# Performance work log

Hardware: AMD Instinct MI355X
Metric: run time of the kernel (lower is better)

The kernel has to match this reference:

```python
import jax, jax.numpy as jnp
import numpy as np

VOCAB = 1024
EMBED = 256
HIDDEN = 512
MAX_LEN = 32
TEMP = 1.0
BATCH = 2048


def setup_inputs() -> dict:
    key = jax.random.key(0)
    ks = jax.random.split(key, 11)
    s = 0.02  # small init scale for weights
    return dict(
        x=jax.random.normal(ks[0], (BATCH, HIDDEN), dtype=jnp.float32),
        gumbel=jax.random.gumbel(ks[1], (MAX_LEN, BATCH, VOCAB), dtype=jnp.float32),
        W_ih=jax.random.normal(ks[2], (4 * HIDDEN, EMBED), dtype=jnp.float32) * s,
        W_hh=jax.random.normal(ks[3], (4 * HIDDEN, HIDDEN), dtype=jnp.float32) * s,
        b_ih=jax.random.normal(ks[4], (4 * HIDDEN,), dtype=jnp.float32) * s,
        b_hh=jax.random.normal(ks[5], (4 * HIDDEN,), dtype=jnp.float32) * s,
        W_out=jax.random.normal(ks[6], (VOCAB, HIDDEN), dtype=jnp.float32) * s,
        b_out=jax.random.normal(ks[7], (VOCAB,), dtype=jnp.float32) * s,
        W_emb=jax.random.normal(ks[8], (EMBED, VOCAB), dtype=jnp.float32) * s,
        b_emb=jax.random.normal(ks[9], (EMBED,), dtype=jnp.float32) * s,
        sos=jax.random.normal(ks[10], (EMBED,), dtype=jnp.float32) * 0.01,
    )


def reference(x, gumbel, W_ih, W_hh, b_ih, b_hh, W_out, b_out, W_emb, b_emb, sos):
    B = x.shape[0]
    h0 = x                                   # prev_hidden = input features
    c0 = jnp.zeros_like(x)
    e0 = jnp.broadcast_to(sos, (B, EMBED))   # SOS embedding

    def step(carry, g):
        h, c, e = carry
        # torch LSTMCell gate order: i, f, g, o
        gates = e @ W_ih.T + b_ih + h @ W_hh.T + b_hh   # [B, 4H]
        i, f, gg, o = jnp.split(gates, 4, axis=-1)
        i = jax.nn.sigmoid(i)
        f = jax.nn.sigmoid(f)
        gg = jnp.tanh(gg)
        o = jax.nn.sigmoid(o)
        c_new = f * c + i * gg
        h_new = o * jnp.tanh(c_new)
        logits = h_new @ W_out.T + b_out                # [B, V]
        # RelaxedOneHotCategorical rsample: softmax((logits + Gumbel)/temp)
        x_s = jax.nn.softmax((logits + g) / TEMP, axis=-1)
        e_new = x_s @ W_emb.T + b_emb                   # [B, E]
        return (h_new, c_new, e_new), x_s

    _, seq = jax.lax.scan(step, (h0, c0, e0), gumbel)   # [L, B, V]
    seq = jnp.transpose(seq, (1, 0, 2))                 # [B, L, V]
    eos = jnp.zeros((B, 1, VOCAB), seq.dtype).at[:, 0, 0].set(1.0)
    return jnp.concatenate([seq, eos], axis=1)          # [B, L+1, V]
```

## Files before the change

### kernel.cpp

```cpp
#include <hip/hip_runtime.h>
#include <hip/hip_bf16.h>

#define B_   2048
#define V_   1024
#define H_   512
#define E_   256
#define L_   32

typedef __attribute__((ext_vector_type(4))) float f32x4;
typedef unsigned short u16;
typedef unsigned int   u32;
typedef unsigned char  u8;
typedef unsigned long long u64;
typedef long long      i64;

__device__ __forceinline__ u32 f32b(float x){ union{float f;u32 u;}v; v.f=x; return v.u; }
__device__ __forceinline__ float bf32(u32 u){ union{float f;u32 u;}v; v.u=u; return v.f; }
__device__ __forceinline__ u16 f2bf(float x) {
    u32 u = f32b(x);
    u32 r = u + 0x7fffu + ((u >> 16) & 1u);
    return (u16)(r >> 16);
}
__device__ __forceinline__ u8 f2e4m3(float x) {
    u32 u = f32b(x);
    u32 s = (u >> 24) & 0x80u;
    u32 a = u & 0x7fffffffu;
    if (a < 0x3c800000u) return (u8)s;
    if (a > 0x43e00000u) a = 0x43e00000u;
    u32 r = a + 0x000fffffu + ((a >> 20) & 1u);
    if (r > 0x43e00000u) r = 0x43e00000u;
    u32 ex = (r >> 23) - 120u;
    u32 mn = (r >> 20) & 7u;
    return (u8)(s | (ex << 3) | mn);
}
__device__ __forceinline__ u8 f2fp8(float x) {
#if __has_builtin(__builtin_amdgcn_cvt_pk_fp8_f32)
    return (u8)(__builtin_amdgcn_cvt_pk_fp8_f32(x, x, 0, false) & 0xff);
#else
    return f2e4m3(x);
#endif
}
__device__ __forceinline__ float sig_(float x)  { return 1.f / (1.f + __expf(-x)); }
__device__ __forceinline__ float tanh_(float x) { return 1.f - 2.f / (__expf(2.f * x) + 1.f); }

__device__ __forceinline__ void ag_st64(void* p, u64 v) {
    __hip_atomic_store((u64*)p, v, __ATOMIC_RELAXED, __HIP_MEMORY_SCOPE_AGENT);
}
__device__ __forceinline__ u64 ag_ld64(const void* p) {
    return __hip_atomic_load((const u64*)p, __ATOMIC_RELAXED, __HIP_MEMORY_SCOPE_AGENT);
}
__device__ __forceinline__ void ag_st32(void* p, u32 v) {
    __hip_atomic_store((u32*)p, v, __ATOMIC_RELAXED, __HIP_MEMORY_SCOPE_AGENT);
}
__device__ __forceinline__ u32 ag_ld32(const void* p) {
    return __hip_atomic_load((const u32*)p, __ATOMIC_RELAXED, __HIP_MEMORY_SCOPE_AGENT);
}

__global__ void prep(const float* __restrict__ W_ih, const float* __restrict__ W_hh,
                     const float* __restrict__ b_ih, const float* __restrict__ b_hh,
                     const float* __restrict__ W_out, const float* __restrict__ W_emb,
                     u8* __restrict__ w1f, u8* __restrict__ wof, u8* __restrict__ wef,
                     float* __restrict__ b1, u32* __restrict__ flg)
{
    int idx = blockIdx.x * 256 + threadIdx.x;
    if (idx < 1572864) {
        int e = idx & 7, l = (idx >> 3) & 63, jj = (idx >> 9) & 1, wv = (idx >> 10) & 7,
            g = (idx >> 13) & 3;
        int rest = idx >> 15;
        int hb = rest / 24, ks = rest % 24;
        int k = ks * 32 + ((l >> 4) << 3) + e;
        int row = g * 512 + hb * 256 + wv * 32 + jj * 16 + (l & 15);
        float v = (k < E_) ? W_ih[row * E_ + k] : W_hh[row * H_ + (k - E_)];
        w1f[idx] = f2e4m3(v * 64.f);
    } else if (idx < 2097152) {
        int j = idx - 1572864;
        int e = j & 7, l = (j >> 3) & 63, jj = (j >> 9) & 1, wv = (j >> 10) & 7,
            vh2 = (j >> 13) & 1, ks = (j >> 14) & 15, hb = j >> 18;
        int k = ks * 32 + ((l >> 4) << 3) + e;
        int v = hb * 512 + vh2 * 256 + wv * 32 + jj * 16 + (l & 15);
        wof[j] = f2e4m3(W_out[v * H_ + k] * 64.f);
    } else if (idx < 2359296) {
        int j = idx - 2097152;
        int e = j & 7, l = (j >> 3) & 63, jj = (j >> 9) & 1, wv = (j >> 10) & 7,
            ksp = (j >> 13) & 15, hb = j >> 17;
        int kv = hb * 512 + ksp * 32 + ((l >> 4) << 3) + e;
        int ce = wv * 32 + jj * 16 + (l & 15);
        wef[j] = f2e4m3(W_emb[ce * V_ + kv] * 64.f);
    } else if (idx < 2361344) {
        int j = idx - 2359296;
        b1[j] = b_ih[j] + b_hh[j];
    } else if (idx < 2365440) {
        flg[idx - 2361344] = 0u;
    }
}

#define AEO   131072u
#define XSO   143488u
#define RMX   151808u
#define RSM   152320u
#define LDS_TOTAL 152832

#define WAITVM_(N) asm volatile("s_waitcnt vmcnt(" #N ")" ::: "memory")
#define WAITVM(N) WAITVM_(N)

typedef const __attribute__((address_space(1))) void* gvp;
typedef __attribute__((address_space(3))) void* svp;

__device__ __forceinline__ void pbar(u32* myf, u32* pef, u32 n, u32 tid) {
    asm volatile("s_waitcnt vmcnt(0)" ::: "memory");
    __syncthreads();
    if (tid == 0) {
        __hip_atomic_fetch_add(myf, 1u, __ATOMIC_RELAXED, __HIP_MEMORY_SCOPE_AGENT);
        while (__hip_atomic_load(pef, __ATOMIC_RELAXED, __HIP_MEMORY_SCOPE_AGENT) < n)
            __builtin_amdgcn_s_sleep(2);
    }
    __syncthreads();
}

__global__ __launch_bounds__(512, 2)
void lstm_fused(const float* __restrict__ x, const float* __restrict__ gum,
                const u8* __restrict__ w1f, const u8* __restrict__ wof,
                const u8* __restrict__ wef, const float* __restrict__ b1,
                const float* __restrict__ b_out, const float* __restrict__ b_emb,
                const float* __restrict__ sos, float* __restrict__ out,
                u8* __restrict__ hx, char* __restrict__ ms, char* __restrict__ ep,
                u32* __restrict__ flg)
{
    extern __shared__ char smem[];

    const u32 tid = threadIdx.x;
    const u32 w   = tid >> 6;
    const u32 l   = tid & 63u;
    const u32 q   = l >> 4;
    const u32 col = l & 15u;

    const u32 bid = blockIdx.x;
    const u32 p   = bid & 127u;
    const u32 hb  = bid >> 7;
    const u32 ph  = 1u - hb;
    const int r0  = (int)(p << 4);

    u32* myf = flg + p * 32u + hb * 16u;
    u32* pef = flg + p * 32u + ph * 16u;
    u32 nbar = 0;

    const u32 wK  = w << 10;
    const u32 lB  = l << 4;
    const u32 l8  = l << 3;
    const u32 q8  = q << 3;
    const u32 colB776 = col * 776u;
    const u32 colB520 = col * 520u;

    const char* w1p = (const char*)w1f + (size_t)hb * 786432u;
    const char* wop = (const char*)wof + (size_t)hb * 262144u;
    const char* wep = (const char*)wef + (size_t)hb * 131072u;

#define ISS(BASE, C) do { u32 _c = (u32)(C); \
    u32 _o = (u32)__builtin_amdgcn_readfirstlane((int)(((_c & 15u) << 13) + wK)); \
    __builtin_amdgcn_global_load_lds((gvp)((BASE) + ((size_t)_c << 13) + wK + lB), \
                                     (svp)(smem + _o), 16, 0, 0); } while (0)

#define CONSA(G, C) { const char* _fb = smem + (((u32)(C) & 15u) << 13) + wK + l8; \
    acc[G][0] = __builtin_amdgcn_mfma_f32_16x16x32_fp8_fp8(a8, *(const i64*)(_fb), acc[G][0], 0, 0, 0); \
    acc[G][1] = __builtin_amdgcn_mfma_f32_16x16x32_fp8_fp8(a8, *(const i64*)(_fb + 512u), acc[G][1], 0, 0, 0); }

#define CONSB(V2, C, A8) { const char* _fb = smem + (((u32)(C) & 15u) << 13) + wK + l8; \
    accB[V2][0] = __builtin_amdgcn_mfma_f32_16x16x32_fp8_fp8(A8, *(const i64*)(_fb), accB[V2][0], 0, 0, 0); \
    accB[V2][1] = __builtin_amdgcn_mfma_f32_16x16x32_fp8_fp8(A8, *(const i64*)(_fb + 512u), accB[V2][1], 0, 0, 0); }

#define CONSC(C) { const char* _fb = smem + (((u32)(C) & 15u) << 13) + wK + l8; \
    i64 _x = *(const i64*)(smem + XSO + colB520 + (((u32)(C)) << 5) + q8); \
    accC[0] = __builtin_amdgcn_mfma_f32_16x16x32_fp8_fp8(_x, *(const i64*)(_fb), accC[0], 0, 0, 0); \
    accC[1] = __builtin_amdgcn_mfma_f32_16x16x32_fp8_fp8(_x, *(const i64*)(_fb + 512u), accC[1], 0, 0, 0); }

    for (u32 i = tid; i < 16u * 512u; i += 512u) {
        u32 row = i >> 9, vl = i & 511u;
        __builtin_nontemporal_store((hb == 0u && vl == 0u) ? 1.f : 0.f,
            &out[((size_t)(r0 + (int)row) * 33 + 32) * V_ + hb * 512u + vl]);
    }
    for (u32 i = tid; i < 16u * 256u; i += 512u) {
        u32 row = i >> 8, k = i & 255u;
        *(u8*)(smem + AEO + row * 776u + k) = f2fp8(sos[k] * 16.f);
    }
    for (u32 i = tid; i < 16u * 512u; i += 512u) {
        u32 row = i >> 9, k = i & 511u;
        *(u8*)(smem + AEO + row * 776u + 256u + k) = f2fp8(x[(r0 + (int)row) * H_ + k] * 16.f);
    }

    float bia[2], bfa[2], bga[2], boa[2];
    #pragma unroll
    for (int jj = 0; jj < 2; ++jj) {
        int jg = (int)(hb * 256u + (w << 5) + ((u32)jj << 4) + col);
        bia[jj] = b1[jg];           bfa[jj] = b1[H_ + jg];
        bga[jj] = b1[2 * H_ + jg];  boa[jj] = b1[3 * H_ + jg];
    }
    float bov[2][2];
    #pragma unroll
    for (int v2 = 0; v2 < 2; ++v2)
        #pragma unroll
        for (int jj = 0; jj < 2; ++jj)
            bov[v2][jj] = b_out[hb * 512u + (u32)v2 * 256u + (w << 5) + ((u32)jj << 4) + col];
    float bem16[2];
    #pragma unroll
    for (int jj = 0; jj < 2; ++jj)
        bem16[jj] = b_emb[(w << 5) + ((u32)jj << 4) + col] * 16.f;

    float creg[2][4];
    #pragma unroll
    for (int jj = 0; jj < 2; ++jj)
        #pragma unroll
        for (int r = 0; r < 4; ++r) creg[jj][r] = 0.f;

    __syncthreads();

    const f32x4 fz = {0.f, 0.f, 0.f, 0.f};
    const float S1 = 1.f / 1024.f;

    ISS(w1p, 0);  ISS(w1p, 1);  ISS(w1p, 2);  ISS(w1p, 3);  ISS(w1p, 4);
    ISS(w1p, 5);  ISS(w1p, 6);  ISS(w1p, 7);  ISS(w1p, 8);  ISS(w1p, 9);
    ISS(w1p, 10); ISS(w1p, 11); ISS(w1p, 12); ISS(w1p, 13); ISS(w1p, 14);

    #pragma unroll 1
    for (int t = 0; t < L_; ++t) {
        f32x4 acc[4][2];
        #pragma unroll
        for (int g = 0; g < 4; ++g) { acc[g][0] = fz; acc[g][1] = fz; }

        #pragma unroll 1
        for (int ks = 0; ks < 20; ++ks) {
            i64 a8 = *(const i64*)(smem + AEO + colB776 + ((u32)ks << 5) + q8);
            int c0 = ks << 2;
            WAITVM(11);
            CONSA(0, c0); CONSA(1, c0 + 1); CONSA(2, c0 + 2); CONSA(3, c0 + 3);
            ISS(w1p, c0 + 15); ISS(w1p, c0 + 16); ISS(w1p, c0 + 17); ISS(w1p, c0 + 18);
        }
        {   i64 a8 = *(const i64*)(smem + AEO + colB776 + (20u << 5) + q8);
            WAITVM(11); CONSA(0, 80); CONSA(1, 81); CONSA(2, 82); CONSA(3, 83); ISS(w1p, 95); }
        {   i64 a8 = *(const i64*)(smem + AEO + colB776 + (21u << 5) + q8);
            WAITVM(8);  CONSA(0, 84); CONSA(1, 85); CONSA(2, 86); CONSA(3, 87); }
        {   i64 a8 = *(const i64*)(smem + AEO + colB776 + (22u << 5) + q8);
            WAITVM(4);  CONSA(0, 88); CONSA(1, 89); CONSA(2, 90); CONSA(3, 91); }
        {   i64 a8 = *(const i64*)(smem + AEO + colB776 + (23u << 5) + q8);
            WAITVM(0);  CONSA(0, 92); CONSA(1, 93); CONSA(2, 94); CONSA(3, 95); }
        __syncthreads();

        #pragma unroll
        for (int jj = 0; jj < 2; ++jj) {
            u32 jg = hb * 256u + (w << 5) + ((u32)jj << 4) + col;
            #pragma unroll
            for (int r = 0; r < 4; ++r) {
                float gi = sig_(acc[0][jj][r] * S1 + bia[jj]);
                float gf = sig_(acc[1][jj][r] * S1 + bfa[jj]);
                float gg = tanh_(acc[2][jj][r] * S1 + bga[jj]);
                float go = sig_(acc[3][jj][r] * S1 + boa[jj]);
                float c  = gf * creg[jj][r] + gi * gg;
                creg[jj][r] = c;
                float h = go * tanh_(c);
                *(u8*)(smem + AEO + ((q << 2) + (u32)r) * 776u + 256u + jg) = f2fp8(h * 16.f);
            }
        }
        __syncthreads();

        {   u32 row = tid >> 5, off = (tid & 31u) << 3;
            u64 v = *(const u64*)(smem + AEO + row * 776u + 256u + hb * 256u + off);
            ag_st64(hx + (size_t)p * 8192u + row * 512u + hb * 256u + off, v);
        }
        ISS(wop, 0);  ISS(wop, 1);  ISS(wop, 2);  ISS(wop, 3);  ISS(wop, 4);
        ISS(wop, 5);  ISS(wop, 6);  ISS(wop, 7);  ISS(wop, 8);  ISS(wop, 9);
        ISS(wop, 10); ISS(wop, 11); ISS(wop, 12); ISS(wop, 13); ISS(wop, 14);
        const float* gt = gum + (size_t)t * (B_ * V_) + (size_t)r0 * V_;
        float gr[2][2][4];
        #pragma unroll
        for (int v2 = 0; v2 < 2; ++v2)
            #pragma unroll
            for (int jj = 0; jj < 2; ++jj) {
                u32 vg = hb * 512u + (u32)v2 * 256u + (w << 5) + ((u32)jj << 4) + col;
                #pragma unroll
                for (int r = 0; r < 4; ++r)
                    gr[v2][jj][r] = __builtin_nontemporal_load(&gt[((q << 2) + (u32)r) * V_ + vg]);
            }
        ++nbar; pbar(myf, pef, nbar, tid);
        {   u32 row = tid >> 5, off = (tid & 31u) << 3;
            u64 v = ag_ld64(hx + (size_t)p * 8192u + row * 512u + ph * 256u + off);
            *(u64*)(smem + AEO + row * 776u + 256u + ph * 256u + off) = v;
        }
        __syncthreads();

        f32x4 accB[2][2];
        accB[0][0] = fz; accB[0][1] = fz; accB[1][0] = fz; accB[1][1] = fz;
        #pragma unroll 1
        for (int g = 0; g < 4; ++g) {
            i64 a80 = *(const i64*)(smem + AEO + colB776 + 256u + (((u32)g << 1) << 5) + q8);
            i64 a81 = *(const i64*)(smem + AEO + colB776 + 256u + ((((u32)g << 1) | 1u) << 5) + q8);
            int c0 = g << 2;
            WAITVM(11);
            CONSB(0, c0, a80); CONSB(1, c0 + 1, a80);
            CONSB(0, c0 + 2, a81); CONSB(1, c0 + 3, a81);
            ISS(wop, c0 + 15); ISS(wop, c0 + 16); ISS(wop, c0 + 17); ISS(wop, c0 + 18);
        }
        {   i64 a80 = *(const i64*)(smem + AEO + colB776 + 256u + (8u << 5) + q8);
            i64 a81 = *(const i64*)(smem + AEO + colB776 + 256u + (9u << 5) + q8);
            WAITVM(11); CONSB(0, 16, a80); CONSB(1, 17, a80); CONSB(0, 18, a81); CONSB(1, 19, a81);
            ISS(wop, 31); }
        {   i64 a80 = *(const i64*)(smem + AEO + colB776 + 256u + (10u << 5) + q8);
            i64 a81 = *(const i64*)(smem + AEO + colB776 + 256u + (11u << 5) + q8);
            WAITVM(8);  CONSB(0, 20, a80); CONSB(1, 21, a80); CONSB(0, 22, a81); CONSB(1, 23, a81); }
        {   i64 a80 = *(const i64*)(smem + AEO + colB776 + 256u + (12u << 5) + q8);
            i64 a81 = *(const i64*)(smem + AEO + colB776 + 256u + (13u << 5) + q8);
            WAITVM(4);  CONSB(0, 24, a80); CONSB(1, 25, a80); CONSB(0, 26, a81); CONSB(1, 27, a81); }
        {   i64 a80 = *(const i64*)(smem + AEO + colB776 + 256u + (14u << 5) + q8);
            i64 a81 = *(const i64*)(smem + AEO + colB776 + 256u + (15u << 5) + q8);
            WAITVM(0);  CONSB(0, 28, a80); CONSB(1, 29, a80); CONSB(0, 30, a81); CONSB(1, 31, a81); }

        float m_loc[4], s_loc[4];
        #pragma unroll
        for (int r = 0; r < 4; ++r) m_loc[r] = -1e30f;
        #pragma unroll
        for (int v2 = 0; v2 < 2; ++v2)
            #pragma unroll
            for (int jj = 0; jj < 2; ++jj)
                #pragma unroll
                for (int r = 0; r < 4; ++r) {
                    float zz = accB[v2][jj][r] * S1 + bov[v2][jj] + gr[v2][jj][r];
                    accB[v2][jj][r] = zz;
                    m_loc[r] = fmaxf(m_loc[r], zz);
                }
        #pragma unroll
        for (int m = 1; m < 16; m <<= 1)
            #pragma unroll
            for (int r = 0; r < 4; ++r) m_loc[r] = fmaxf(m_loc[r], __shfl_xor(m_loc[r], m, 64));
        if (col == 0) {
            #pragma unroll
            for (int r = 0; r < 4; ++r)
                *(float*)(smem + RMX + ((((q << 2) + (u32)r) << 3) + w) * 4u) = m_loc[r];
        }
        __syncthreads();
        #pragma unroll
        for (int r = 0; r < 4; ++r) {
            float mm = -1e30f;
            #pragma unroll
            for (int ww = 0; ww < 8; ++ww)
                mm = fmaxf(mm, *(const float*)(smem + RMX + ((((q << 2) + (u32)r) << 3) + (u32)ww) * 4u));
            m_loc[r] = mm;
        }
        ISS(wep, 0);  ISS(wep, 1);  ISS(wep, 2);  ISS(wep, 3);  ISS(wep, 4);
        ISS(wep, 5);  ISS(wep, 6);  ISS(wep, 7);  ISS(wep, 8);  ISS(wep, 9);
        ISS(wep, 10); ISS(wep, 11); ISS(wep, 12); ISS(wep, 13); ISS(wep, 14);
        float ps[4] = {0.f, 0.f, 0.f, 0.f};
        #pragma unroll
        for (int v2 = 0; v2 < 2; ++v2)
            #pragma unroll
            for (int jj = 0; jj < 2; ++jj) {
                u32 vl = (u32)v2 * 256u + (w << 5) + ((u32)jj << 4) + col;
                #pragma unroll
                for (int r = 0; r < 4; ++r) {
                    float Ee = __expf(accB[v2][jj][r] - m_loc[r]);
                    accB[v2][jj][r] = Ee;
                    ps[r] += Ee;
                    *(u8*)(smem + XSO + ((q << 2) + (u32)r) * 520u + vl) = f2fp8(Ee * 256.f);
                }
            }
        #pragma unroll
        for (int m = 1; m < 16; m <<= 1)
            #pragma unroll
            for (int r = 0; r < 4; ++r) ps[r] += __shfl_xor(ps[r], m, 64);
        if (col == 0) {
            #pragma unroll
            for (int r = 0; r < 4; ++r)
                *(float*)(smem + RSM + ((((q << 2) + (u32)r) << 3) + w) * 4u) = ps[r];
        }
        __syncthreads();
        #pragma unroll
        for (int r = 0; r < 4; ++r) {
            float ss = 0.f;
            #pragma unroll
            for (int ww = 0; ww < 8; ++ww)
                ss += *(const float*)(smem + RSM + ((((q << 2) + (u32)r) << 3) + (u32)ww) * 4u);
            s_loc[r] = ss;
        }

        f32x4 accC[2];
        accC[0] = fz; accC[1] = fz;
        WAITVM(11); CONSC(0);  CONSC(1);  CONSC(2);  CONSC(3);  ISS(wep, 15);
        WAITVM(8);  CONSC(4);  CONSC(5);  CONSC(6);  CONSC(7);
        WAITVM(4);  CONSC(8);  CONSC(9);  CONSC(10); CONSC(11);
        WAITVM(0);  CONSC(12); CONSC(13); CONSC(14); CONSC(15);

        float part[2][4];
        #pragma unroll
        for (int jj = 0; jj < 2; ++jj)
            #pragma unroll
            for (int r = 0; r < 4; ++r)
                part[jj][r] = accC[jj][r] * (16.f / 16384.f);
        if (w == 0 && col == 0) {
            #pragma unroll
            for (int r = 0; r < 4; ++r) {
                u64 v = ((u64)f32b(s_loc[r]) << 32) | (u64)f32b(m_loc[r]);
                ag_st64(ms + (size_t)p * 256u + hb * 128u + (((q << 2) + (u32)r) << 3), v);
            }
        }
        #pragma unroll
        for (int r = 0; r < 4; ++r) {
            u32 row = (q << 2) + (u32)r;
            u32 pv = (u32)f2bf(part[0][r]) | ((u32)f2bf(part[1][r]) << 16);
            ag_st32(ep + (size_t)p * 16384u + hb * 8192u + (((row << 3) + w) << 6) + (col << 2), pv);
        }
        ISS(w1p, 0);  ISS(w1p, 1);  ISS(w1p, 2);  ISS(w1p, 3);  ISS(w1p, 4);
        ISS(w1p, 5);  ISS(w1p, 6);  ISS(w1p, 7);  ISS(w1p, 8);  ISS(w1p, 9);
        ISS(w1p, 10); ISS(w1p, 11); ISS(w1p, 12); ISS(w1p, 13); ISS(w1p, 14);
        ++nbar; pbar(myf, pef, nbar, tid);

        float f0a[4], f1a[4], inva[4];
        #pragma unroll
        for (int r = 0; r < 4; ++r) {
            u64 v = ag_ld64(ms + (size_t)p * 256u + ph * 128u + (((q << 2) + (u32)r) << 3));
            float m_p = bf32((u32)v), s_p = bf32((u32)(v >> 32));
            float mg = fmaxf(m_loc[r], m_p);
            float f0 = __expf(m_loc[r] - mg), f1 = __expf(m_p - mg);
            float inv = 1.f / (s_loc[r] * f0 + s_p * f1);
            f0a[r] = f0; f1a[r] = f1; inva[r] = inv;
        }
        #pragma unroll
        for (int v2 = 0; v2 < 2; ++v2)
            #pragma unroll
            for (int jj = 0; jj < 2; ++jj) {
                u32 vg = hb * 512u + (u32)v2 * 256u + (w << 5) + ((u32)jj << 4) + col;
                #pragma unroll
                for (int r = 0; r < 4; ++r)
                    __builtin_nontemporal_store(accB[v2][jj][r] * f0a[r] * inva[r],
                        &out[((size_t)(r0 + (int)((q << 2) + (u32)r)) * 33 + t) * V_ + vg]);
            }
        #pragma unroll
        for (int r = 0; r < 4; ++r) {
            u32 row = (q << 2) + (u32)r;
            u32 pv = ag_ld32(ep + (size_t)p * 16384u + ph * 8192u + (((row << 3) + w) << 6) + (col << 2));
            #pragma unroll
            for (int jj = 0; jj < 2; ++jj) {
                float pe = bf32(((pv >> (16 * jj)) & 0xffffu) << 16);
                float e16 = (part[jj][r] * f0a[r] + pe * f1a[r]) * inva[r] + bem16[jj];
                *(u8*)(smem + AEO + row * 776u + (w << 5) + ((u32)jj << 4) + col) = f2fp8(e16);
            }
        }
        __syncthreads();
    }
#undef ISS
#undef CONSA
#undef CONSB
#undef CONSC
}

extern "C" void kernel_launch(void* const* d_in, const int* in_sizes, int n_in,
                              void* d_out, int out_size, void* d_ws, size_t ws_size,
                              hipStream_t stream) {
    const float* x     = (const float*)d_in[0];
    const float* gum   = (const float*)d_in[1];
    const float* W_ih  = (const float*)d_in[2];
    const float* W_hh  = (const float*)d_in[3];
    const float* b_ih  = (const float*)d_in[4];
    const float* b_hh  = (const float*)d_in[5];
    const float* W_out = (const float*)d_in[6];
    const float* b_out = (const float*)d_in[7];
    const float* W_emb = (const float*)d_in[8];
    const float* b_emb = (const float*)d_in[9];
    const float* sos   = (const float*)d_in[10];
    float* out = (float*)d_out;

    char* ws = (char*)d_ws;
    u8*    w1f = (u8*)(ws);
    u8*    wof = (u8*)(ws + 1572864);
    u8*    wef = (u8*)(ws + 2097152);
    float* b1  = (float*)(ws + 2359296);
    u32*   flg = (u32*)(ws + 2367488);
    u8*    hx  = (u8*)(ws + 2383872);
    char*  ms  = (char*)(ws + 3432448);
    char*  ep  = (char*)(ws + 3465216);

    hipFuncSetAttribute((const void*)lstm_fused,
                        hipFuncAttributeMaxDynamicSharedMemorySize, LDS_TOTAL);

    prep<<<9240, 256, 0, stream>>>(W_ih, W_hh, b_ih, b_hh, W_out, W_emb,
                                   w1f, wof, wef, b1, flg);
    lstm_fused<<<256, 512, LDS_TOTAL, stream>>>(x, gum, w1f, wof, wef, b1,
                                                b_out, b_emb, sos, out,
                                                hx, ms, ep, flg);
}
```

Measured before the change: 868.1 us.

## Split output projection into own-half and peer-half phases around pair barrier

The output-logits GEMM over the hidden dimension is split so the block first consumes the W_out chunks matching its own locally computed hidden half before the inter-block pair barrier. Only after that does it wait for and import the peer's hidden half and finish the peer chunks. The barrier wait now uses a partial vmcnt so outstanding weight prefetches are not drained. Scheduling barriers pin the issue order. This overlaps barrier latency with MFMA work, at the cost of reordered weight chunks that must match the preprocessed layout, and a relaxed wait that must still cover the global stores before signalling.

```diff
diff --git a/kernel.cpp b/kernel.cpp
--- a/kernel.cpp
+++ b/kernel.cpp
@@ -102,20 +102,10 @@
 
 #define WAITVM_(N) asm volatile("s_waitcnt vmcnt(" #N ")" ::: "memory")
 #define WAITVM(N) WAITVM_(N)
+#define SCHEDB() __builtin_amdgcn_sched_barrier(0)
 
 typedef const __attribute__((address_space(1))) void* gvp;
 typedef __attribute__((address_space(3))) void* svp;
-
-__device__ __forceinline__ void pbar(u32* myf, u32* pef, u32 n, u32 tid) {
-    asm volatile("s_waitcnt vmcnt(0)" ::: "memory");
-    __syncthreads();
-    if (tid == 0) {
-        __hip_atomic_fetch_add(myf, 1u, __ATOMIC_RELAXED, __HIP_MEMORY_SCOPE_AGENT);
-        while (__hip_atomic_load(pef, __ATOMIC_RELAXED, __HIP_MEMORY_SCOPE_AGENT) < n)
-            __builtin_amdgcn_s_sleep(2);
-    }
-    __syncthreads();
-}
 
 __global__ __launch_bounds__(512, 2)
 void lstm_fused(const float* __restrict__ x, const float* __restrict__ gum,
@@ -150,23 +140,46 @@
     const u32 q8  = q << 3;
     const u32 colB776 = col * 776u;
     const u32 colB520 = col * 520u;
+    const u32 hb16 = hb << 4, ph16 = ph << 4;
+    const u32 hOwnOff  = 256u + (hb << 8);
+    const u32 hPeerOff = 256u + (ph << 8);
 
     const char* w1p = (const char*)w1f + (size_t)hb * 786432u;
     const char* wop = (const char*)wof + (size_t)hb * 262144u;
     const char* wep = (const char*)wef + (size_t)hb * 131072u;
+
+#define PBAR(N) do { WAITVM(N); __syncthreads(); \
+    if (tid == 0) { \
+        __hip_atomic_fetch_add(myf, 1u, __ATOMIC_RELAXED, __HIP_MEMORY_SCOPE_AGENT); \
+        while (__hip_atomic_load(pef, __ATOMIC_RELAXED, __HIP_MEMORY_SCOPE_AGENT) < nbar) \
+            __builtin_amdgcn_s_sleep(2); \
+    } \
+    __syncthreads(); } while (0)
 
 #define ISS(BASE, C) do { u32 _c = (u32)(C); \
     u32 _o = (u32)__builtin_amdgcn_readfirstlane((int)(((_c & 15u) << 13) + wK)); \
     __builtin_amdgcn_global_load_lds((gvp)((BASE) + ((size_t)_c << 13) + wK + lB), \
                                      (svp)(smem + _o), 16, 0, 0); } while (0)
+#define ISSB_OWN(I) do { u32 _c = hb16 + (u32)(I); \
+    u32 _o = (u32)__builtin_amdgcn_readfirstlane((int)((((u32)(I) & 15u) << 13) + wK)); \
+    __builtin_amdgcn_global_load_lds((gvp)(wop + ((size_t)_c << 13) + wK + lB), \
+                                     (svp)(smem + _o), 16, 0, 0); } while (0)
+#define ISSB_P(I) do { u32 _c = ph16 + (u32)(I); \
+    u32 _o = (u32)__builtin_amdgcn_readfirstlane((int)((((u32)(I) & 15u) << 13) + wK)); \
+    __builtin_amdgcn_global_load_lds((gvp)(wop + ((size_t)_c << 13) + wK + lB), \
+                                     (svp)(smem + _o), 16, 0, 0); } while (0)
 
 #define CONSA(G, C) { const char* _fb = smem + (((u32)(C) & 15u) << 13) + wK + l8; \
     acc[G][0] = __builtin_amdgcn_mfma_f32_16x16x32_fp8_fp8(a8, *(const i64*)(_fb), acc[G][0], 0, 0, 0); \
     acc[G][1] = __builtin_amdgcn_mfma_f32_16x16x32_fp8_fp8(a8, *(const i64*)(_fb + 512u), acc[G][1], 0, 0, 0); }
 
-#define CONSB(V2, C, A8) { const char* _fb = smem + (((u32)(C) & 15u) << 13) + wK + l8; \
+#define CONSB(V2, SLOT, A8) { const char* _fb = smem + (((u32)(SLOT) & 15u) << 13) + wK + l8; \
     accB[V2][0] = __builtin_amdgcn_mfma_f32_16x16x32_fp8_fp8(A8, *(const i64*)(_fb), accB[V2][0], 0, 0, 0); \
     accB[V2][1] = __builtin_amdgcn_mfma_f32_16x16x32_fp8_fp8(A8, *(const i64*)(_fb + 512u), accB[V2][1], 0, 0, 0); }
+
+#define BGRP(I, NW, HOFF) { \
+    i64 a8 = *(const i64*)(smem + AEO + colB776 + (HOFF) + ((u32)(I) << 5) + q8); \
+    WAITVM(NW); CONSB(0, 2*(I), a8); CONSB(1, 2*(I) + 1, a8); }
 
 #define CONSC(C) { const char* _fb = smem + (((u32)(C) & 15u) << 13) + wK + l8; \
     i64 _x = *(const i64*)(smem + XSO + colB520 + (((u32)(C)) << 5) + q8); \
@@ -265,9 +278,12 @@
             u64 v = *(const u64*)(smem + AEO + row * 776u + 256u + hb * 256u + off);
             ag_st64(hx + (size_t)p * 8192u + row * 512u + hb * 256u + off, v);
         }
-        ISS(wop, 0);  ISS(wop, 1);  ISS(wop, 2);  ISS(wop, 3);  ISS(wop, 4);
-        ISS(wop, 5);  ISS(wop, 6);  ISS(wop, 7);  ISS(wop, 8);  ISS(wop, 9);
-        ISS(wop, 10); ISS(wop, 11); ISS(wop, 12); ISS(wop, 13); ISS(wop, 14);
+        SCHEDB();
+        ISSB_OWN(0);  ISSB_OWN(1);  ISSB_OWN(2);  ISSB_OWN(3);
+        ISSB_OWN(4);  ISSB_OWN(5);  ISSB_OWN(6);  ISSB_OWN(7);
+        ISSB_OWN(8);  ISSB_OWN(9);  ISSB_OWN(10); ISSB_OWN(11);
+        ISSB_OWN(12); ISSB_OWN(13); ISSB_OWN(14); ISSB_OWN(15);
+        SCHEDB();
         const float* gt = gum + (size_t)t * (B_ * V_) + (size_t)r0 * V_;
         float gr[2][2][4];
         #pragma unroll
@@ -279,38 +295,36 @@
                 for (int r = 0; r < 4; ++r)
                     gr[v2][jj][r] = __builtin_nontemporal_load(&gt[((q << 2) + (u32)r) * V_ + vg]);
             }
-        ++nbar; pbar(myf, pef, nbar, tid);
-        {   u32 row = tid >> 5, off = (tid & 31u) << 3;
-            u64 v = ag_ld64(hx + (size_t)p * 8192u + row * 512u + ph * 256u + off);
-            *(u64*)(smem + AEO + row * 776u + 256u + ph * 256u + off) = v;
-        }
-        __syncthreads();
+        SCHEDB();
 
         f32x4 accB[2][2];
         accB[0][0] = fz; accB[0][1] = fz; accB[1][0] = fz; accB[1][1] = fz;
-        #pragma unroll 1
-        for (int g = 0; g < 4; ++g) {
-            i64 a80 = *(const i64*)(smem + AEO + colB776 + 256u + (((u32)g << 1) << 5) + q8);
-            i64 a81 = *(const i64*)(smem + AEO + colB776 + 256u + ((((u32)g << 1) | 1u) << 5) + q8);
-            int c0 = g << 2;
-            WAITVM(11);
-            CONSB(0, c0, a80); CONSB(1, c0 + 1, a80);
-            CONSB(0, c0 + 2, a81); CONSB(1, c0 + 3, a81);
-            ISS(wop, c0 + 15); ISS(wop, c0 + 16); ISS(wop, c0 + 17); ISS(wop, c0 + 18);
-        }
-        {   i64 a80 = *(const i64*)(smem + AEO + colB776 + 256u + (8u << 5) + q8);
-            i64 a81 = *(const i64*)(smem + AEO + colB776 + 256u + (9u << 5) + q8);
-            WAITVM(11); CONSB(0, 16, a80); CONSB(1, 17, a80); CONSB(0, 18, a81); CONSB(1, 19, a81);
-            ISS(wop, 31); }
-        {   i64 a80 = *(const i64*)(smem + AEO + colB776 + 256u + (10u << 5) + q8);
-            i64 a81 = *(const i64*)(smem + AEO + colB776 + 256u + (11u << 5) + q8);
-            WAITVM(8);  CONSB(0, 20, a80); CONSB(1, 21, a80); CONSB(0, 22, a81); CONSB(1, 23, a81); }
-        {   i64 a80 = *(const i64*)(smem + AEO + colB776 + 256u + (12u << 5) + q8);
-            i64 a81 = *(const i64*)(smem + AEO + colB776 + 256u + (13u << 5) + q8);
-            WAITVM(4);  CONSB(0, 24, a80); CONSB(1, 25, a80); CONSB(0, 26, a81); CONSB(1, 27, a81); }
-        {   i64 a80 = *(const i64*)(smem + AEO + colB776 + 256u + (14u << 5) + q8);
-            i64 a81 = *(const i64*)(smem + AEO + colB776 + 256u + (15u << 5) + q8);
-            WAITVM(0);  CONSB(0, 28, a80); CONSB(1, 29, a80); CONSB(0, 30, a81); CONSB(1, 31, a81); }
+        BGRP(0, 44, hOwnOff); BGRP(1, 40, hOwnOff);
+        BGRP(2, 36, hOwnOff); BGRP(3, 32, hOwnOff);
+        BGRP(4, 28, hOwnOff); BGRP(5, 24, hOwnOff);
+        BGRP(6, 20, hOwnOff); BGRP(7, 16, hOwnOff);
+
+        ++nbar; PBAR(16);
+
+        u64 himp;
+        {   u32 row = tid >> 5, off = (tid & 31u) << 3;
+            himp = ag_ld64(hx + (size_t)p * 8192u + row * 512u + ph * 256u + off);
+        }
+        SCHEDB();
+        ISSB_P(0);  ISSB_P(1);  ISSB_P(2);  ISSB_P(3);
+        ISSB_P(4);  ISSB_P(5);  ISSB_P(6);  ISSB_P(7);
+        ISSB_P(8);  ISSB_P(9);  ISSB_P(10); ISSB_P(11);
+        ISSB_P(12); ISSB_P(13); ISSB_P(14); ISSB_P(15);
+        SCHEDB();
+        {   u32 row = tid >> 5, off = (tid & 31u) << 3;
+            *(u64*)(smem + AEO + row * 776u + 256u + ph * 256u + off) = himp;
+        }
+        __syncthreads();
+
+        BGRP(0, 28, hPeerOff); BGRP(1, 24, hPeerOff);
+        BGRP(2, 20, hPeerOff); BGRP(3, 16, hPeerOff);
+        BGRP(4, 12, hPeerOff); BGRP(5, 8, hPeerOff);
+        BGRP(6, 4, hPeerOff);  BGRP(7, 0, hPeerOff);
 
         float m_loc[4], s_loc[4];
         #pragma unroll
@@ -405,10 +419,12 @@
             u32 pv = (u32)f2bf(part[0][r]) | ((u32)f2bf(part[1][r]) << 16);
             ag_st32(ep + (size_t)p * 16384u + hb * 8192u + (((row << 3) + w) << 6) + (col << 2), pv);
         }
+        SCHEDB();
         ISS(w1p, 0);  ISS(w1p, 1);  ISS(w1p, 2);  ISS(w1p, 3);  ISS(w1p, 4);
         ISS(w1p, 5);  ISS(w1p, 6);  ISS(w1p, 7);  ISS(w1p, 8);  ISS(w1p, 9);
         ISS(w1p, 10); ISS(w1p, 11); ISS(w1p, 12); ISS(w1p, 13); ISS(w1p, 14);
-        ++nbar; pbar(myf, pef, nbar, tid);
+        SCHEDB();
+        ++nbar; PBAR(30);
 
         float f0a[4], f1a[4], inva[4];
         #pragma unroll
@@ -444,9 +460,13 @@
         __syncthreads();
     }
 #undef ISS
+#undef ISSB_OWN
+#undef ISSB_P
 #undef CONSA
 #undef CONSB
+#undef BGRP
 #undef CONSC
+#undef PBAR
 }
 
 extern "C" void kernel_launch(void* const* d_in, const int* in_sizes, int n_in,
```

After: 990.8 us. 1.14x slower.

## Stream fp8 weights directly into registers instead of staging through LDS

Applied to the files above, without the earlier changes.

Replaces the global_load_lds ring buffer (16 slots of 8KB in LDS) with a six-deep register ring of 16-byte weight loads that feed the MFMAs directly. LDS drops from about 150KB to about 21KB and becomes static shared memory. The prep kernel's weight layout is reordered so that each lane reads a contiguous 16-byte chunk. The Wout prefetch now starts before the cross-block barrier, so the hidden-state exchange overlaps with those loads. The trade-off is higher register pressure and reliance on the compiler's vmcnt scheduling instead of explicit waits.

```diff
diff --git a/kernel.cpp b/kernel.cpp
--- a/kernel.cpp
+++ b/kernel.cpp
@@ -8,6 +8,7 @@
 #define L_   32
 
 typedef __attribute__((ext_vector_type(4))) float f32x4;
+typedef __attribute__((ext_vector_type(2))) long i64x2;
 typedef unsigned short u16;
 typedef unsigned int   u32;
 typedef unsigned char  u8;
@@ -62,60 +63,56 @@
                      u8* __restrict__ w1f, u8* __restrict__ wof, u8* __restrict__ wef,
                      float* __restrict__ b1, u32* __restrict__ flg)
 {
-    int idx = blockIdx.x * 256 + threadIdx.x;
-    if (idx < 1572864) {
-        int e = idx & 7, l = (idx >> 3) & 63, jj = (idx >> 9) & 1, wv = (idx >> 10) & 7,
-            g = (idx >> 13) & 3;
-        int rest = idx >> 15;
-        int hb = rest / 24, ks = rest % 24;
-        int k = ks * 32 + ((l >> 4) << 3) + e;
-        int row = g * 512 + hb * 256 + wv * 32 + jj * 16 + (l & 15);
+    u32 idx = blockIdx.x * 256 + threadIdx.x;
+    if (idx < 1572864u) {
+        u32 hb = idx / 786432u;
+        u32 r  = idx - hb * 786432u;
+        u32 ks = r >> 15;
+        u32 r2 = r & 32767u;
+        u32 g = r2 >> 13, wv = (r2 >> 10) & 7u, l = (r2 >> 4) & 63u,
+            jj = (r2 >> 3) & 1u, e = r2 & 7u;
+        u32 k = ks * 32u + ((l >> 4) << 3) + e;
+        u32 row = g * 512u + hb * 256u + wv * 32u + jj * 16u + (l & 15u);
         float v = (k < E_) ? W_ih[row * E_ + k] : W_hh[row * H_ + (k - E_)];
         w1f[idx] = f2e4m3(v * 64.f);
-    } else if (idx < 2097152) {
-        int j = idx - 1572864;
-        int e = j & 7, l = (j >> 3) & 63, jj = (j >> 9) & 1, wv = (j >> 10) & 7,
-            vh2 = (j >> 13) & 1, ks = (j >> 14) & 15, hb = j >> 18;
-        int k = ks * 32 + ((l >> 4) << 3) + e;
-        int v = hb * 512 + vh2 * 256 + wv * 32 + jj * 16 + (l & 15);
+    } else if (idx < 2097152u) {
+        u32 j = idx - 1572864u;
+        u32 hb = j >> 18;
+        u32 r  = j & 262143u;
+        u32 ks = r >> 14;
+        u32 r2 = r & 16383u;
+        u32 vh2 = r2 >> 13;
+        u32 r3 = r2 & 8191u;
+        u32 wv = r3 >> 10, l = (r3 >> 4) & 63u, jj = (r3 >> 3) & 1u, e = r3 & 7u;
+        u32 k = ks * 32u + ((l >> 4) << 3) + e;
+        u32 v = hb * 512u + vh2 * 256u + wv * 32u + jj * 16u + (l & 15u);
         wof[j] = f2e4m3(W_out[v * H_ + k] * 64.f);
-    } else if (idx < 2359296) {
-        int j = idx - 2097152;
-        int e = j & 7, l = (j >> 3) & 63, jj = (j >> 9) & 1, wv = (j >> 10) & 7,
-            ksp = (j >> 13) & 15, hb = j >> 17;
-        int kv = hb * 512 + ksp * 32 + ((l >> 4) << 3) + e;
-        int ce = wv * 32 + jj * 16 + (l & 15);
+    } else if (idx < 2359296u) {
+        u32 j = idx - 2097152u;
+        u32 hb = j >> 17;
+        u32 r  = j & 131071u;
+        u32 ksp = r >> 13;
+        u32 r2 = r & 8191u;
+        u32 wv = r2 >> 10, l = (r2 >> 4) & 63u, jj = (r2 >> 3) & 1u, e = r2 & 7u;
+        u32 kv = hb * 512u + ksp * 32u + ((l >> 4) << 3) + e;
+        u32 ce = wv * 32u + jj * 16u + (l & 15u);
         wef[j] = f2e4m3(W_emb[ce * V_ + kv] * 64.f);
-    } else if (idx < 2361344) {
-        int j = idx - 2359296;
+    } else if (idx < 2361344u) {
+        u32 j = idx - 2359296u;
         b1[j] = b_ih[j] + b_hh[j];
-    } else if (idx < 2365440) {
-        flg[idx - 2361344] = 0u;
-    }
-}
-
-#define AEO   131072u
-#define XSO   143488u
-#define RMX   151808u
-#define RSM   152320u
-#define LDS_TOTAL 152832
+    } else if (idx < 2365440u) {
+        flg[idx - 2361344u] = 0u;
+    }
+}
+
+#define AEO   0u
+#define XSO   12416u
+#define RMX   20736u
+#define RSM   21248u
+#define LDS_TOTAL 21760
 
 #define WAITVM_(N) asm volatile("s_waitcnt vmcnt(" #N ")" ::: "memory")
 #define WAITVM(N) WAITVM_(N)
-
-typedef const __attribute__((address_space(1))) void* gvp;
-typedef __attribute__((address_space(3))) void* svp;
-
-__device__ __forceinline__ void pbar(u32* myf, u32* pef, u32 n, u32 tid) {
-    asm volatile("s_waitcnt vmcnt(0)" ::: "memory");
-    __syncthreads();
-    if (tid == 0) {
-        __hip_atomic_fetch_add(myf, 1u, __ATOMIC_RELAXED, __HIP_MEMORY_SCOPE_AGENT);
-        while (__hip_atomic_load(pef, __ATOMIC_RELAXED, __HIP_MEMORY_SCOPE_AGENT) < n)
-            __builtin_amdgcn_s_sleep(2);
-    }
-    __syncthreads();
-}
 
 __global__ __launch_bounds__(512, 2)
 void lstm_fused(const float* __restrict__ x, const float* __restrict__ gum,
@@ -126,7 +123,7 @@
                 u8* __restrict__ hx, char* __restrict__ ms, char* __restrict__ ep,
                 u32* __restrict__ flg)
 {
-    extern __shared__ char smem[];
+    __shared__ __align__(16) char smem[LDS_TOTAL];
 
     const u32 tid = threadIdx.x;
     const u32 w   = tid >> 6;
@@ -144,34 +141,26 @@
     u32* pef = flg + p * 32u + ph * 16u;
     u32 nbar = 0;
 
-    const u32 wK  = w << 10;
-    const u32 lB  = l << 4;
-    const u32 l8  = l << 3;
+    const u32 wvl = (w << 10) + (l << 4);
     const u32 q8  = q << 3;
     const u32 colB776 = col * 776u;
     const u32 colB520 = col * 520u;
 
-    const char* w1p = (const char*)w1f + (size_t)hb * 786432u;
-    const char* wop = (const char*)wof + (size_t)hb * 262144u;
-    const char* wep = (const char*)wef + (size_t)hb * 131072u;
-
-#define ISS(BASE, C) do { u32 _c = (u32)(C); \
-    u32 _o = (u32)__builtin_amdgcn_readfirstlane((int)(((_c & 15u) << 13) + wK)); \
-    __builtin_amdgcn_global_load_lds((gvp)((BASE) + ((size_t)_c << 13) + wK + lB), \
-                                     (svp)(smem + _o), 16, 0, 0); } while (0)
-
-#define CONSA(G, C) { const char* _fb = smem + (((u32)(C) & 15u) << 13) + wK + l8; \
-    acc[G][0] = __builtin_amdgcn_mfma_f32_16x16x32_fp8_fp8(a8, *(const i64*)(_fb), acc[G][0], 0, 0, 0); \
-    acc[G][1] = __builtin_amdgcn_mfma_f32_16x16x32_fp8_fp8(a8, *(const i64*)(_fb + 512u), acc[G][1], 0, 0, 0); }
-
-#define CONSB(V2, C, A8) { const char* _fb = smem + (((u32)(C) & 15u) << 13) + wK + l8; \
-    accB[V2][0] = __builtin_amdgcn_mfma_f32_16x16x32_fp8_fp8(A8, *(const i64*)(_fb), accB[V2][0], 0, 0, 0); \
-    accB[V2][1] = __builtin_amdgcn_mfma_f32_16x16x32_fp8_fp8(A8, *(const i64*)(_fb + 512u), accB[V2][1], 0, 0, 0); }
-
-#define CONSC(C) { const char* _fb = smem + (((u32)(C) & 15u) << 13) + wK + l8; \
-    i64 _x = *(const i64*)(smem + XSO + colB520 + (((u32)(C)) << 5) + q8); \
-    accC[0] = __builtin_amdgcn_mfma_f32_16x16x32_fp8_fp8(_x, *(const i64*)(_fb), accC[0], 0, 0, 0); \
-    accC[1] = __builtin_amdgcn_mfma_f32_16x16x32_fp8_fp8(_x, *(const i64*)(_fb + 512u), accC[1], 0, 0, 0); }
+    const char* w1q = (const char*)w1f + (size_t)hb * 786432u;
+    const char* woq = (const char*)wof + (size_t)hb * 262144u;
+    const char* weq = (const char*)wef + (size_t)hb * 131072u;
+
+#define PBAR() do { WAITVM(0); __syncthreads(); \
+    if (tid == 0) { \
+        __hip_atomic_fetch_add(myf, 1u, __ATOMIC_RELAXED, __HIP_MEMORY_SCOPE_AGENT); \
+        while (__hip_atomic_load(pef, __ATOMIC_RELAXED, __HIP_MEMORY_SCOPE_AGENT) < nbar) \
+            __builtin_amdgcn_s_sleep(2); \
+    } \
+    __syncthreads(); } while (0)
+
+#define LDW1(U) (*(const i64x2*)(w1q + (size_t)((U) * 8192u) + wvl))
+#define LDWO(U) (*(const i64x2*)(woq + (size_t)((U) * 8192u) + wvl))
+#define LDWE(U) (*(const i64x2*)(weq + (size_t)((U) * 8192u) + wvl))
 
     for (u32 i = tid; i < 16u * 512u; i += 512u) {
         u32 row = i >> 9, vl = i & 511u;
@@ -215,10 +204,11 @@
 
     const f32x4 fz = {0.f, 0.f, 0.f, 0.f};
     const float S1 = 1.f / 1024.f;
-
-    ISS(w1p, 0);  ISS(w1p, 1);  ISS(w1p, 2);  ISS(w1p, 3);  ISS(w1p, 4);
-    ISS(w1p, 5);  ISS(w1p, 6);  ISS(w1p, 7);  ISS(w1p, 8);  ISS(w1p, 9);
-    ISS(w1p, 10); ISS(w1p, 11); ISS(w1p, 12); ISS(w1p, 13); ISS(w1p, 14);
+    const float CSC = 16.f / 16384.f;
+
+    i64x2 rg[6];
+    #pragma unroll
+    for (int s = 0; s < 6; ++s) rg[s] = LDW1(s);
 
     #pragma unroll 1
     for (int t = 0; t < L_; ++t) {
@@ -226,22 +216,17 @@
         #pragma unroll
         for (int g = 0; g < 4; ++g) { acc[g][0] = fz; acc[g][1] = fz; }
 
-        #pragma unroll 1
-        for (int ks = 0; ks < 20; ++ks) {
+        #pragma unroll
+        for (int ks = 0; ks < 24; ++ks) {
             i64 a8 = *(const i64*)(smem + AEO + colB776 + ((u32)ks << 5) + q8);
-            int c0 = ks << 2;
-            WAITVM(11);
-            CONSA(0, c0); CONSA(1, c0 + 1); CONSA(2, c0 + 2); CONSA(3, c0 + 3);
-            ISS(w1p, c0 + 15); ISS(w1p, c0 + 16); ISS(w1p, c0 + 17); ISS(w1p, c0 + 18);
-        }
-        {   i64 a8 = *(const i64*)(smem + AEO + colB776 + (20u << 5) + q8);
-            WAITVM(11); CONSA(0, 80); CONSA(1, 81); CONSA(2, 82); CONSA(3, 83); ISS(w1p, 95); }
-        {   i64 a8 = *(const i64*)(smem + AEO + colB776 + (21u << 5) + q8);
-            WAITVM(8);  CONSA(0, 84); CONSA(1, 85); CONSA(2, 86); CONSA(3, 87); }
-        {   i64 a8 = *(const i64*)(smem + AEO + colB776 + (22u << 5) + q8);
-            WAITVM(4);  CONSA(0, 88); CONSA(1, 89); CONSA(2, 90); CONSA(3, 91); }
-        {   i64 a8 = *(const i64*)(smem + AEO + colB776 + (23u << 5) + q8);
-            WAITVM(0);  CONSA(0, 92); CONSA(1, 93); CONSA(2, 94); CONSA(3, 95); }
+            #pragma unroll
+            for (int g = 0; g < 4; ++g) {
+                const int u = ks * 4 + g, s = u % 6;
+                acc[g][0] = __builtin_amdgcn_mfma_f32_16x16x32_fp8_fp8(a8, rg[s][0], acc[g][0], 0, 0, 0);
+                acc[g][1] = __builtin_amdgcn_mfma_f32_16x16x32_fp8_fp8(a8, rg[s][1], acc[g][1], 0, 0, 0);
+                if (u + 6 < 96) rg[s] = LDW1(u + 6);
+            }
+        }
         __syncthreads();
 
         #pragma unroll
@@ -265,9 +250,16 @@
             u64 v = *(const u64*)(smem + AEO + row * 776u + 256u + hb * 256u + off);
             ag_st64(hx + (size_t)p * 8192u + row * 512u + hb * 256u + off, v);
         }
-        ISS(wop, 0);  ISS(wop, 1);  ISS(wop, 2);  ISS(wop, 3);  ISS(wop, 4);
-        ISS(wop, 5);  ISS(wop, 6);  ISS(wop, 7);  ISS(wop, 8);  ISS(wop, 9);
-        ISS(wop, 10); ISS(wop, 11); ISS(wop, 12); ISS(wop, 13); ISS(wop, 14);
+        i64x2 rb[6];
+        #pragma unroll
+        for (int s = 0; s < 6; ++s) rb[s] = LDWO(s);
+        ++nbar; PBAR();
+        {   u32 row = tid >> 5, off = (tid & 31u) << 3;
+            u64 v = ag_ld64(hx + (size_t)p * 8192u + row * 512u + ph * 256u + off);
+            *(u64*)(smem + AEO + row * 776u + 256u + ph * 256u + off) = v;
+        }
+        __syncthreads();
+
         const float* gt = gum + (size_t)t * (B_ * V_) + (size_t)r0 * V_;
         float gr[2][2][4];
         #pragma unroll
@@ -279,38 +271,20 @@
                 for (int r = 0; r < 4; ++r)
                     gr[v2][jj][r] = __builtin_nontemporal_load(&gt[((q << 2) + (u32)r) * V_ + vg]);
             }
-        ++nbar; pbar(myf, pef, nbar, tid);
-        {   u32 row = tid >> 5, off = (tid & 31u) << 3;
-            u64 v = ag_ld64(hx + (size_t)p * 8192u + row * 512u + ph * 256u + off);
-            *(u64*)(smem + AEO + row * 776u + 256u + ph * 256u + off) = v;
-        }
-        __syncthreads();
 
         f32x4 accB[2][2];
         accB[0][0] = fz; accB[0][1] = fz; accB[1][0] = fz; accB[1][1] = fz;
-        #pragma unroll 1
-        for (int g = 0; g < 4; ++g) {
-            i64 a80 = *(const i64*)(smem + AEO + colB776 + 256u + (((u32)g << 1) << 5) + q8);
-            i64 a81 = *(const i64*)(smem + AEO + colB776 + 256u + ((((u32)g << 1) | 1u) << 5) + q8);
-            int c0 = g << 2;
-            WAITVM(11);
-            CONSB(0, c0, a80); CONSB(1, c0 + 1, a80);
-            CONSB(0, c0 + 2, a81); CONSB(1, c0 + 3, a81);
-            ISS(wop, c0 + 15); ISS(wop, c0 + 16); ISS(wop, c0 + 17); ISS(wop, c0 + 18);
-        }
-        {   i64 a80 = *(const i64*)(smem + AEO + colB776 + 256u + (8u << 5) + q8);
-            i64 a81 = *(const i64*)(smem + AEO + colB776 + 256u + (9u << 5) + q8);
-            WAITVM(11); CONSB(0, 16, a80); CONSB(1, 17, a80); CONSB(0, 18, a81); CONSB(1, 19, a81);
-            ISS(wop, 31); }
-        {   i64 a80 = *(const i64*)(smem + AEO + colB776 + 256u + (10u << 5) + q8);
-            i64 a81 = *(const i64*)(smem + AEO + colB776 + 256u + (11u << 5) + q8);
-            WAITVM(8);  CONSB(0, 20, a80); CONSB(1, 21, a80); CONSB(0, 22, a81); CONSB(1, 23, a81); }
-        {   i64 a80 = *(const i64*)(smem + AEO + colB776 + 256u + (12u << 5) + q8);
-            i64 a81 = *(const i64*)(smem + AEO + colB776 + 256u + (13u << 5) + q8);
-            WAITVM(4);  CONSB(0, 24, a80); CONSB(1, 25, a80); CONSB(0, 26, a81); CONSB(1, 27, a81); }
-        {   i64 a80 = *(const i64*)(smem + AEO + colB776 + 256u + (14u << 5) + q8);
-            i64 a81 = *(const i64*)(smem + AEO + colB776 + 256u + (15u << 5) + q8);
-            WAITVM(0);  CONSB(0, 28, a80); CONSB(1, 29, a80); CONSB(0, 30, a81); CONSB(1, 31, a81); }
+        #pragma unroll
+        for (int ks = 0; ks < 16; ++ks) {
+            i64 a8 = *(const i64*)(smem + AEO + colB776 + 256u + ((u32)ks << 5) + q8);
+            #pragma unroll
+            for (int v2 = 0; v2 < 2; ++v2) {
+                const int u = ks * 2 + v2, s = u % 6;
+                accB[v2][0] = __builtin_amdgcn_mfma_f32_16x16x32_fp8_fp8(a8, rb[s][0], accB[v2][0], 0, 0, 0);
+                accB[v2][1] = __builtin_amdgcn_mfma_f32_16x16x32_fp8_fp8(a8, rb[s][1], accB[v2][1], 0, 0, 0);
+                if (u + 6 < 32) rb[s] = LDWO(u + 6);
+            }
+        }
 
         float m_loc[4], s_loc[4];
         #pragma unroll
@@ -343,9 +317,9 @@
                 mm = fmaxf(mm, *(const float*)(smem + RMX + ((((q << 2) + (u32)r) << 3) + (u32)ww) * 4u));
             m_loc[r] = mm;
         }
-        ISS(wep, 0);  ISS(wep, 1);  ISS(wep, 2);  ISS(wep, 3);  ISS(wep, 4);
-        ISS(wep, 5);  ISS(wep, 6);  ISS(wep, 7);  ISS(wep, 8);  ISS(wep, 9);
-        ISS(wep, 10); ISS(wep, 11); ISS(wep, 12); ISS(wep, 13); ISS(wep, 14);
+        i64x2 rc[6];
+        #pragma unroll
+        for (int s = 0; s < 6; ++s) rc[s] = LDWE(s);
         float ps[4] = {0.f, 0.f, 0.f, 0.f};
         #pragma unroll
         for (int v2 = 0; v2 < 2; ++v2)
@@ -381,17 +355,15 @@
 
         f32x4 accC[2];
         accC[0] = fz; accC[1] = fz;
-        WAITVM(11); CONSC(0);  CONSC(1);  CONSC(2);  CONSC(3);  ISS(wep, 15);
-        WAITVM(8);  CONSC(4);  CONSC(5);  CONSC(6);  CONSC(7);
-        WAITVM(4);  CONSC(8);  CONSC(9);  CONSC(10); CONSC(11);
-        WAITVM(0);  CONSC(12); CONSC(13); CONSC(14); CONSC(15);
-
-        float part[2][4];
-        #pragma unroll
-        for (int jj = 0; jj < 2; ++jj)
-            #pragma unroll
-            for (int r = 0; r < 4; ++r)
-                part[jj][r] = accC[jj][r] * (16.f / 16384.f);
+        #pragma unroll
+        for (int u = 0; u < 16; ++u) {
+            const int s = u % 6;
+            i64 xv = *(const i64*)(smem + XSO + colB520 + ((u32)u << 5) + q8);
+            accC[0] = __builtin_amdgcn_mfma_f32_16x16x32_fp8_fp8(xv, rc[s][0], accC[0], 0, 0, 0);
+            accC[1] = __builtin_amdgcn_mfma_f32_16x16x32_fp8_fp8(xv, rc[s][1], accC[1], 0, 0, 0);
+            if (u + 6 < 16) rc[s] = LDWE(u + 6);
+        }
+
         if (w == 0 && col == 0) {
             #pragma unroll
             for (int r = 0; r < 4; ++r) {
@@ -402,13 +374,12 @@
         #pragma unroll
         for (int r = 0; r < 4; ++r) {
             u32 row = (q << 2) + (u32)r;
-            u32 pv = (u32)f2bf(part[0][r]) | ((u32)f2bf(part[1][r]) << 16);
+            u32 pv = (u32)f2bf(accC[0][r] * CSC) | ((u32)f2bf(accC[1][r] * CSC) << 16);
             ag_st32(ep + (size_t)p * 16384u + hb * 8192u + (((row << 3) + w) << 6) + (col << 2), pv);
         }
-        ISS(w1p, 0);  ISS(w1p, 1);  ISS(w1p, 2);  ISS(w1p, 3);  ISS(w1p, 4);
-        ISS(w1p, 5);  ISS(w1p, 6);  ISS(w1p, 7);  ISS(w1p, 8);  ISS(w1p, 9);
-        ISS(w1p, 10); ISS(w1p, 11); ISS(w1p, 12); ISS(w1p, 13); ISS(w1p, 14);
-        ++nbar; pbar(myf, pef, nbar, tid);
+        #pragma unroll
+        for (int s = 0; s < 6; ++s) rg[s] = LDW1(s);
+        ++nbar; PBAR();
 
         float f0a[4], f1a[4], inva[4];
         #pragma unroll
@@ -437,16 +408,16 @@
             #pragma unroll
             for (int jj = 0; jj < 2; ++jj) {
                 float pe = bf32(((pv >> (16 * jj)) & 0xffffu) << 16);
-                float e16 = (part[jj][r] * f0a[r] + pe * f1a[r]) * inva[r] + bem16[jj];
+                float e16 = (accC[jj][r] * CSC * f0a[r] + pe * f1a[r]) * inva[r] + bem16[jj];
                 *(u8*)(smem + AEO + row * 776u + (w << 5) + ((u32)jj << 4) + col) = f2fp8(e16);
             }
         }
         __syncthreads();
     }
-#undef ISS
-#undef CONSA
-#undef CONSB
-#undef CONSC
+#undef PBAR
+#undef LDW1
+#undef LDWO
+#undef LDWE
 }
 
 extern "C" void kernel_launch(void* const* d_in, const int* in_sizes, int n_in,
@@ -475,12 +446,9 @@
     char*  ms  = (char*)(ws + 3432448);
     char*  ep  = (char*)(ws + 3465216);
 
-    hipFuncSetAttribute((const void*)lstm_fused,
-                        hipFuncAttributeMaxDynamicSharedMemorySize, LDS_TOTAL);
-
     prep<<<9240, 256, 0, stream>>>(W_ih, W_hh, b_ih, b_hh, W_out, W_emb,
                                    w1f, wof, wef, b1, flg);
-    lstm_fused<<<256, 512, LDS_TOTAL, stream>>>(x, gum, w1f, wof, wef, b1,
-                                                b_out, b_emb, sos, out,
-                                                hx, ms, ep, flg);
-}
+    lstm_fused<<<256, 512, 0, stream>>>(x, gum, w1f, wof, wef, b1,
+                                        b_out, b_emb, sos, out,
+                                        hx, ms, ep, flg);
+}
```

After: 1.986 ms. +128.8%, slower.
